# Performance work log

Hardware: AMD Instinct MI355X
Metric: run time of the kernel (lower is better)

The kernel has to match this reference:

```python
import jax, jax.numpy as jnp
import numpy as np

N = 50000
E = 800000
NFEAT = 128
NHID = 128


def _glorot(key, shape):
    fan = shape[0] + shape[-1]
    s = jnp.sqrt(6.0 / fan)
    return jax.random.uniform(key, shape, jnp.float32, -s, s)


def setup_inputs() -> dict:
    key = jax.random.key(0)
    ks = jax.random.split(key, 8)
    x = jax.random.normal(ks[0], (N, NFEAT), jnp.float32)
    edge_index = jax.random.randint(ks[1], (2, E), 0, N, jnp.int64)
    return {
        "x": x,
        "edge_index": edge_index,
        "Wl1": _glorot(ks[2], (NFEAT, NHID)),
        "bl1": jnp.zeros((NHID,), jnp.float32),
        "Wr1": _glorot(ks[3], (NFEAT, NHID)),
        "br1": jnp.zeros((NHID,), jnp.float32),
        "att1": _glorot(ks[4], (NHID,)),
        "b1": jnp.zeros((NHID,), jnp.float32),
        "Wl2": _glorot(ks[5], (NHID, NHID)),
        "bl2": jnp.zeros((NHID,), jnp.float32),
        "Wr2": _glorot(ks[6], (NHID, NHID)),
        "br2": jnp.zeros((NHID,), jnp.float32),
        "att2": _glorot(ks[7], (NHID,)),
        "b2": jnp.zeros((NHID,), jnp.float32),
    }


def gatv2_conv(x, src, dst, Wl, bl, Wr, br, att, bias, neg_slope=0.2):
    # PyG GATv2Conv, heads=1, concat=True, add_self_loops handled by caller.
    xl = x @ Wl + bl                      # [N, H] source transform
    xr = x @ Wr + br                      # [N, H] target transform
    e = jax.nn.leaky_relu(xl[src] + xr[dst], neg_slope) @ att  # [E']
    # segment softmax over incoming edges per destination node
    m = jax.ops.segment_max(e, dst, num_segments=x.shape[0])
    w = jnp.exp(e - m[dst])
    denom = jax.ops.segment_sum(w, dst, num_segments=x.shape[0])
    alpha = w / denom[dst]                # [E']
    out = jax.ops.segment_sum(alpha[:, None] * xl[src], dst,
                              num_segments=x.shape[0])
    return out + bias


def reference(x, edge_index, Wl1, bl1, Wr1, br1, att1, b1,
              Wl2, bl2, Wr2, br2, att2, b2):
    n = x.shape[0]
    loop = jnp.arange(n, dtype=edge_index.dtype)
    src = jnp.concatenate([edge_index[0], loop])  # add self loops (PyG default)
    dst = jnp.concatenate([edge_index[1], loop])
    h = gatv2_conv(x, src, dst, Wl1, bl1, Wr1, br1, att1, b1)
    h = jax.nn.leaky_relu(h, 0.01)  # F.leaky_relu default slope
    out = gatv2_conv(h, src, dst, Wl2, bl2, Wr2, br2, att2, b2)
    return out
```

## Files before the change

### kernel.cpp

```cpp
#include <hip/hip_runtime.h>
#include <math.h>

#define HD 128
#define CHUNK 2048
#define MAXBINS 512
#define NPB 128
#define CAP 3072

typedef __attribute__((ext_vector_type(8))) short bf16x8;
typedef __attribute__((ext_vector_type(4))) float f32x4;
typedef __attribute__((ext_vector_type(2))) float f32x2;

__device__ __forceinline__ unsigned short f2bf(float f) {
    unsigned int u = __float_as_uint(f);
    u += 0x7FFFu + ((u >> 16) & 1u);
    return (unsigned short)(u >> 16);
}
__device__ __forceinline__ float bflo(unsigned int p) {
    return __uint_as_float(p << 16);
}
__device__ __forceinline__ float bfhi(unsigned int p) {
    return __uint_as_float(p & 0xFFFF0000u);
}
__device__ __forceinline__ f32x2 bfpair(unsigned int p) {
    f32x2 r;
    r.x = __uint_as_float(p << 16);
    r.y = __uint_as_float(p & 0xFFFF0000u);
    return r;
}

__global__ __launch_bounds__(256) void wprep_kernel(
    const float* __restrict__ W0, const float* __restrict__ W1,
    const float* __restrict__ W2, const float* __restrict__ W3,
    uint4* __restrict__ T0, uint4* __restrict__ T1,
    uint4* __restrict__ T2, uint4* __restrict__ T3,
    int* __restrict__ binCursor, int nbins)
{
    int g = blockIdx.x * 256 + threadIdx.x;
    if (g < nbins) binCursor[g] = g * CAP;

    const int m = blockIdx.x >> 3;
    const int s = (blockIdx.x & 7) * 256 + threadIdx.x;
    const float* W = (m == 0) ? W0 : (m == 1) ? W1 : (m == 2) ? W2 : W3;
    uint4* T = (m == 0) ? T0 : (m == 1) ? T1 : (m == 2) ? T2 : T3;

    const int l = s & 63;
    const int ckk = s >> 6;
    const int kk = ckk & 3;
    const int c = ckk >> 2;
    const int k0 = kk * 32 + (l >> 4) * 8;
    const int col = c * 16 + (l & 15);

    unsigned int b[8];
    #pragma unroll
    for (int j = 0; j < 8; ++j)
        b[j] = f2bf(W[(size_t)(k0 + j) * HD + col]);
    uint4 o;
    o.x = b[0] | (b[1] << 16);
    o.y = b[2] | (b[3] << 16);
    o.z = b[4] | (b[5] << 16);
    o.w = b[6] | (b[7] << 16);
    T[s] = o;
}

__global__ __launch_bounds__(512, 4) void gemm_mfma_kernel(
    const float* __restrict__ X,
    const uint4* __restrict__ WlF, const float* __restrict__ bl,
    const uint4* __restrict__ WrF, const float* __restrict__ br,
    unsigned short* __restrict__ Ylb, unsigned short* __restrict__ Yrb, int n)
{
    __shared__ unsigned short xs[64 * HD];
    __shared__ uint4 bsl[2048];
    __shared__ uint4 bsr[2048];
    const int row0 = blockIdx.x * 64;
    const int tid = threadIdx.x;
    const int lane = tid & 63;
    const int wv = tid >> 6;

    {
        const float4* Xv = (const float4*)(X + (size_t)row0 * HD);
        #pragma unroll
        for (int i = 0; i < 4; ++i) {
            int idx = tid + i * 512;
            int row = idx >> 5;
            int c4 = idx & 31;
            float4 v = make_float4(0.f, 0.f, 0.f, 0.f);
            if (row0 + row < n) v = Xv[idx];
            ushort4 b;
            b.x = f2bf(v.x); b.y = f2bf(v.y); b.z = f2bf(v.z); b.w = f2bf(v.w);
            int byteoff = row * 256 + ((c4 * 8) ^ ((row & 7) << 4));
            *(ushort4*)((char*)xs + byteoff) = b;
        }
    }
    #pragma unroll
    for (int i = 0; i < 4; ++i) {
        bsl[tid + i * 512] = WlF[tid + i * 512];
        bsr[tid + i * 512] = WrF[tid + i * 512];
    }
    __syncthreads();

    const int r15 = lane & 15;
    const int kg = lane >> 4;
    const int mrow = (wv & 3) * 16 + r15;
    const int cbase = (wv >> 2) * 4;
    const int abase = mrow * 256;
    const int aswz = (mrow & 7) << 4;

    bf16x8 af[4];
    #pragma unroll
    for (int kk = 0; kk < 4; ++kk)
        af[kk] = *(const bf16x8*)((const char*)xs + abase + ((kk * 64 + kg * 16) ^ aswz));

    f32x4 accl[4], accr[4];
    #pragma unroll
    for (int i = 0; i < 4; ++i) {
        accl[i] = (f32x4){0.f, 0.f, 0.f, 0.f};
        accr[i] = (f32x4){0.f, 0.f, 0.f, 0.f};
    }

    #pragma unroll
    for (int kk = 0; kk < 4; ++kk) {
        #pragma unroll
        for (int c = 0; c < 4; ++c) {
            bf16x8 bfl = *(const bf16x8*)&bsl[((cbase + c) * 4 + kk) * 64 + lane];
            accl[c] = __builtin_amdgcn_mfma_f32_16x16x32_bf16(af[kk], bfl, accl[c], 0, 0, 0);
            bf16x8 bfr = *(const bf16x8*)&bsr[((cbase + c) * 4 + kk) * 64 + lane];
            accr[c] = __builtin_amdgcn_mfma_f32_16x16x32_bf16(af[kk], bfr, accr[c], 0, 0, 0);
        }
    }

    const int orow0 = row0 + (wv & 3) * 16 + kg * 4;
    #pragma unroll
    for (int c = 0; c < 4; ++c) {
        const int col = (cbase + c) * 16 + r15;
        const float bLv = bl[col];
        const float bRv = br[col];
        #pragma unroll
        for (int r = 0; r < 4; ++r) {
            int row = orow0 + r;
            if (row < n) {
                Ylb[(size_t)row * HD + col] = f2bf(accl[c][r] + bLv);
                Yrb[(size_t)row * HD + col] = f2bf(accr[c][r] + bRv);
            }
        }
    }
}

__global__ __launch_bounds__(256) void bin_scatter_kernel(
    const int* __restrict__ ei, int* __restrict__ binCursor,
    unsigned int* __restrict__ binned, int nE, int nTot, int nbins)
{
    __shared__ int hist[MAXBINS];
    __shared__ int base[MAXBINS];
    for (int i = threadIdx.x; i < nbins; i += 256) hist[i] = 0;
    __syncthreads();
    const int e0 = blockIdx.x * CHUNK;
    const int e1 = min(e0 + CHUNK, nTot);
    for (int e = e0 + threadIdx.x; e < e1; e += 256) {
        int d = (e < nE) ? ei[nE + e] : (e - nE);
        atomicAdd(&hist[d >> 7], 1);
    }
    __syncthreads();
    for (int b = threadIdx.x; b < nbins; b += 256) {
        int c = hist[b];
        base[b] = c ? atomicAdd(&binCursor[b], c) : 0;
        hist[b] = 0;
    }
    __syncthreads();
    for (int e = e0 + threadIdx.x; e < e1; e += 256) {
        int s, d;
        if (e < nE) { s = ei[e]; d = ei[nE + e]; }
        else        { s = e - nE; d = s; }
        int b = d >> 7;
        int r = atomicAdd(&hist[b], 1);
        binned[base[b] + r] = (unsigned int)s | ((unsigned int)(d & (NPB - 1)) << 16);
    }
}

__global__ __launch_bounds__(256) void bin_csr_kernel(
    const int* __restrict__ binCursor, const unsigned int* __restrict__ binned,
    int* __restrict__ rowstart, int* __restrict__ rowlen,
    int* __restrict__ csr_src, int n)
{
    __shared__ int hist[NPB];
    __shared__ int cur[NPB];
    __shared__ int sm[256];
    const int b = blockIdx.x;
    const int tid = threadIdx.x;
    const int lo = b * CAP;
    const int hi = binCursor[b];

    if (tid < NPB) hist[tid] = 0;
    __syncthreads();
    for (int e = lo + tid; e < hi; e += 256)
        atomicAdd(&hist[(binned[e] >> 16) & (NPB - 1)], 1);
    __syncthreads();
    const int c = (tid < NPB) ? hist[tid] : 0;
    const int rl = (c + 3) & ~3;
    sm[tid] = rl;
    __syncthreads();
    #pragma unroll
    for (int off = 1; off < 256; off <<= 1) {
        int v = (tid >= off) ? sm[tid - off] : 0;
        __syncthreads();
        sm[tid] += v;
        __syncthreads();
    }
    const int excl = sm[tid] - rl;
    if (tid < NPB) {
        cur[tid] = excl;
        int node = b * NPB + tid;
        if (node < n) { rowstart[node] = lo + excl; rowlen[node] = c; }
    }
    __syncthreads();
    for (int e = lo + tid; e < hi; e += 256) {
        unsigned int p = binned[e];
        int r = atomicAdd(&cur[(p >> 16) & (NPB - 1)], 1);
        csr_src[lo + r] = (int)(p & 0xFFFFu);
    }
    __syncthreads();
    if (tid < NPB) {
        int node = b * NPB + tid;
        if (node < n) {
            for (int r2 = excl + c; r2 < excl + rl; ++r2) csr_src[lo + r2] = node;
        }
    }
    int total = sm[255];
    if (tid < 64) csr_src[lo + total + tid] = 0;
}

__device__ __forceinline__ void gat4(
    uint2 u0, uint2 u1, uint2 u2, uint2 u3,
    const f32x2 xrA, const f32x2 xrB, const f32x2 attA, const f32x2 attB,
    int k0, int len,
    float& den, f32x2& accA, f32x2& accB)
{
    f32x2 c0a = bfpair(u0.x), c0b = bfpair(u0.y);
    f32x2 c1a = bfpair(u1.x), c1b = bfpair(u1.y);
    f32x2 c2a = bfpair(u2.x), c2b = bfpair(u2.y);
    f32x2 c3a = bfpair(u3.x), c3b = bfpair(u3.y);

    f32x2 v, tp;
    float t0, t1, t2, t3;
    v = c0a + xrA; v = __builtin_elementwise_max(v, v * 0.2f); tp = v * attA;
    v = c0b + xrB; v = __builtin_elementwise_max(v, v * 0.2f); tp += v * attB;
    t0 = tp.x + tp.y;
    v = c1a + xrA; v = __builtin_elementwise_max(v, v * 0.2f); tp = v * attA;
    v = c1b + xrB; v = __builtin_elementwise_max(v, v * 0.2f); tp += v * attB;
    t1 = tp.x + tp.y;
    v = c2a + xrA; v = __builtin_elementwise_max(v, v * 0.2f); tp = v * attA;
    v = c2b + xrB; v = __builtin_elementwise_max(v, v * 0.2f); tp += v * attB;
    t2 = tp.x + tp.y;
    v = c3a + xrA; v = __builtin_elementwise_max(v, v * 0.2f); tp = v * attA;
    v = c3b + xrB; v = __builtin_elementwise_max(v, v * 0.2f); tp += v * attB;
    t3 = tp.x + tp.y;

    #pragma unroll
    for (int off = 16; off >= 1; off >>= 1) {
        t0 += __shfl_xor(t0, off);
        t1 += __shfl_xor(t1, off);
        t2 += __shfl_xor(t2, off);
        t3 += __shfl_xor(t3, off);
    }

    if (k0 + 0 >= len) t0 = -1e30f;
    if (k0 + 1 >= len) t1 = -1e30f;
    if (k0 + 2 >= len) t2 = -1e30f;
    if (k0 + 3 >= len) t3 = -1e30f;

    float p0 = exp2f(t0);
    float p1 = exp2f(t1);
    float p2 = exp2f(t2);
    float p3 = exp2f(t3);
    den += (p0 + p1) + (p2 + p3);
    accA += p0 * c0a + p1 * c1a + p2 * c2a + p3 * c3a;
    accB += p0 * c0b + p1 * c1b + p2 * c2b + p3 * c3b;
}

__global__ __launch_bounds__(256) void fused_gat_kernel(
    const int* __restrict__ rowstart, const int* __restrict__ rowlen,
    const int* __restrict__ csr_src,
    const unsigned short* __restrict__ xlb, const unsigned short* __restrict__ xrb,
    const float* __restrict__ att, const float* __restrict__ bias,
    float* __restrict__ out, int n, int doAct)
{
    const int wid  = blockIdx.x * 4 + (threadIdx.x >> 6);
    const int lane = threadIdx.x & 63;
    const int d    = wid * 2 + (lane >> 5);
    const int fl   = (lane & 31) * 4;

    const float LOG2E = 1.44269504088896f;
    const float4 attf = *(const float4*)(att + fl);
    const f32x2 attA = (f32x2){attf.x * LOG2E, attf.y * LOG2E};
    const f32x2 attB = (f32x2){attf.z * LOG2E, attf.w * LOG2E};

    f32x2 xrA = (f32x2){0.f, 0.f}, xrB = (f32x2){0.f, 0.f};
    int rp = 0, len = 0;
    if (d < n) {
        uint2 xru = *(const uint2*)(xrb + (size_t)d * HD + fl);
        xrA = bfpair(xru.x);
        xrB = bfpair(xru.y);
        rp  = rowstart[d];
        len = rowlen[d];
    }
    const int rl = (len + 3) & ~3;
    const int ml = max(rl, __shfl_xor(rl, 32));

    float den = 0.f;
    f32x2 accA = (f32x2){0.f, 0.f}, accB = (f32x2){0.f, 0.f};

    const unsigned short* xfl = xlb + fl;

    uint2 a0, a1, a2, a3, b0, b1, b2, b3;
    {
        int i0 = csr_src[rp + 0], i1 = csr_src[rp + 1];
        int i2 = csr_src[rp + 2], i3 = csr_src[rp + 3];
        int j0 = csr_src[rp + 4], j1 = csr_src[rp + 5];
        int j2 = csr_src[rp + 6], j3 = csr_src[rp + 7];
        a0 = *(const uint2*)(xfl + (size_t)i0 * HD);
        a1 = *(const uint2*)(xfl + (size_t)i1 * HD);
        a2 = *(const uint2*)(xfl + (size_t)i2 * HD);
        a3 = *(const uint2*)(xfl + (size_t)i3 * HD);
        b0 = *(const uint2*)(xfl + (size_t)j0 * HD);
        b1 = *(const uint2*)(xfl + (size_t)j1 * HD);
        b2 = *(const uint2*)(xfl + (size_t)j2 * HD);
        b3 = *(const uint2*)(xfl + (size_t)j3 * HD);
    }

    for (int k0 = 0; k0 < ml; k0 += 8) {
        uint2 u0 = a0, u1 = a1, u2 = a2, u3 = a3;
        int kn = k0 + 8;
        if (kn < ml) {
            int i0 = csr_src[rp + kn + 0], i1 = csr_src[rp + kn + 1];
            int i2 = csr_src[rp + kn + 2], i3 = csr_src[rp + kn + 3];
            a0 = *(const uint2*)(xfl + (size_t)i0 * HD);
            a1 = *(const uint2*)(xfl + (size_t)i1 * HD);
            a2 = *(const uint2*)(xfl + (size_t)i2 * HD);
            a3 = *(const uint2*)(xfl + (size_t)i3 * HD);
        }
        gat4(u0, u1, u2, u3, xrA, xrB, attA, attB, k0, len, den, accA, accB);

        if (k0 + 4 < ml) {
            uint2 v0 = b0, v1 = b1, v2 = b2, v3 = b3;
            int km = k0 + 12;
            if (km < ml) {
                int j0 = csr_src[rp + km + 0], j1 = csr_src[rp + km + 1];
                int j2 = csr_src[rp + km + 2], j3 = csr_src[rp + km + 3];
                b0 = *(const uint2*)(xfl + (size_t)j0 * HD);
                b1 = *(const uint2*)(xfl + (size_t)j1 * HD);
                b2 = *(const uint2*)(xfl + (size_t)j2 * HD);
                b3 = *(const uint2*)(xfl + (size_t)j3 * HD);
            }
            gat4(v0, v1, v2, v3, xrA, xrB, attA, attB, k0 + 4, len, den, accA, accB);
        }
    }

    if (d < n) {
        const float4 bv = *(const float4*)(bias + fl);
        float inv = 1.f / den;
        float o0 = accA.x * inv + bv.x;
        float o1 = accA.y * inv + bv.y;
        float o2 = accB.x * inv + bv.z;
        float o3 = accB.y * inv + bv.w;
        if (doAct) {
            o0 = (o0 > 0.f) ? o0 : 0.01f * o0;
            o1 = (o1 > 0.f) ? o1 : 0.01f * o1;
            o2 = (o2 > 0.f) ? o2 : 0.01f * o2;
            o3 = (o3 > 0.f) ? o3 : 0.01f * o3;
        }
        *(float4*)(out + (size_t)d * HD + fl) = make_float4(o0, o1, o2, o3);
    }
}

extern "C" void kernel_launch(void* const* d_in, const int* in_sizes, int n_in,
                              void* d_out, int out_size, void* d_ws, size_t ws_size,
                              hipStream_t stream)
{
    const float* x    = (const float*)d_in[0];
    const int*   ei   = (const int*)d_in[1];
    const float* Wl1  = (const float*)d_in[2];
    const float* bl1  = (const float*)d_in[3];
    const float* Wr1  = (const float*)d_in[4];
    const float* br1  = (const float*)d_in[5];
    const float* att1 = (const float*)d_in[6];
    const float* b1   = (const float*)d_in[7];
    const float* Wl2  = (const float*)d_in[8];
    const float* bl2  = (const float*)d_in[9];
    const float* Wr2  = (const float*)d_in[10];
    const float* br2  = (const float*)d_in[11];
    const float* att2 = (const float*)d_in[12];
    const float* b2   = (const float*)d_in[13];

    const int n    = in_sizes[0] / HD;
    const int E    = in_sizes[1] / 2;
    const int nTot = E + n;
    const int nbins = (n + NPB - 1) / NPB;

    char* ws = (char*)d_ws;
    const size_t feat_bytes = (size_t)n * HD * sizeof(float);
    const size_t bf_bytes   = ((size_t)n * HD * 2 + 511) & ~(size_t)511;
    const size_t wt_bytes   = ((size_t)HD * HD * 2 + 511) & ~(size_t)511;
    auto alignup = [](size_t v) { return (v + 511) & ~(size_t)511; };
    unsigned short* xlb = (unsigned short*)ws; ws += bf_bytes;
    unsigned short* xrb = (unsigned short*)ws; ws += bf_bytes;
    float* h  = (float*)ws;          ws += feat_bytes;
    uint4* wlF1 = (uint4*)ws; ws += wt_bytes;
    uint4* wrF1 = (uint4*)ws; ws += wt_bytes;
    uint4* wlF2 = (uint4*)ws; ws += wt_bytes;
    uint4* wrF2 = (uint4*)ws; ws += wt_bytes;
    int* binCursor = (int*)ws;       ws += alignup((size_t)nbins * 4);
    int* rowstart  = (int*)ws;       ws += alignup((size_t)n * 4);
    int* rowlen    = (int*)ws;       ws += alignup((size_t)n * 4);
    unsigned int* binned = (unsigned int*)ws; ws += alignup((size_t)nbins * CAP * 4);
    int* csr_src   = (int*)ws;       ws += alignup((size_t)nbins * CAP * 4);

    float* out = (float*)d_out;

    const int nChunk = (nTot + CHUNK - 1) / CHUNK;
    dim3 gb(512); dim3 gg((n + 63) / 64);
    dim3 fb(256); dim3 fg((n + 7) / 8);

    wprep_kernel<<<32, 256, 0, stream>>>(Wl1, Wr1, Wl2, Wr2, wlF1, wrF1, wlF2, wrF2,
                                         binCursor, nbins);
    bin_scatter_kernel<<<nChunk, 256, 0, stream>>>(ei, binCursor, binned, E, nTot, nbins);
    bin_csr_kernel<<<nbins, 256, 0, stream>>>(binCursor, binned, rowstart, rowlen, csr_src, n);

    gemm_mfma_kernel<<<gg, gb, 0, stream>>>(x, wlF1, bl1, wrF1, br1, xlb, xrb, n);
    fused_gat_kernel<<<fg, fb, 0, stream>>>(rowstart, rowlen, csr_src, xlb, xrb, att1, b1, h, n, 1);

    gemm_mfma_kernel<<<gg, gb, 0, stream>>>(h, wlF2, bl2, wrF2, br2, xlb, xrb, n);
    fused_gat_kernel<<<fg, fb, 0, stream>>>(rowstart, rowlen, csr_src, xlb, xrb, att2, b2, out, n, 0);
}
```

Baseline: 159.4 us.

## Sort nodes by degree within each bin to balance half-wave pairs

```diff
diff --git a/kernel.cpp b/kernel.cpp
--- a/kernel.cpp
+++ b/kernel.cpp
@@ -15,12 +15,6 @@
     unsigned int u = __float_as_uint(f);
     u += 0x7FFFu + ((u >> 16) & 1u);
     return (unsigned short)(u >> 16);
-}
-__device__ __forceinline__ float bflo(unsigned int p) {
-    return __uint_as_float(p << 16);
-}
-__device__ __forceinline__ float bfhi(unsigned int p) {
-    return __uint_as_float(p & 0xFFFF0000u);
 }
 __device__ __forceinline__ f32x2 bfpair(unsigned int p) {
     f32x2 r;
@@ -180,11 +174,12 @@
 __global__ __launch_bounds__(256) void bin_csr_kernel(
     const int* __restrict__ binCursor, const unsigned int* __restrict__ binned,
     int* __restrict__ rowstart, int* __restrict__ rowlen,
-    int* __restrict__ csr_src, int n)
+    int* __restrict__ csr_src, int* __restrict__ pairs, int n)
 {
     __shared__ int hist[NPB];
     __shared__ int cur[NPB];
     __shared__ int sm[256];
+    __shared__ unsigned int srt[NPB];
     const int b = blockIdx.x;
     const int tid = threadIdx.x;
     const int lo = b * CAP;
@@ -198,6 +193,7 @@
     const int c = (tid < NPB) ? hist[tid] : 0;
     const int rl = (c + 3) & ~3;
     sm[tid] = rl;
+    if (tid < NPB) srt[tid] = ((unsigned int)rl << 7) | (unsigned int)tid;
     __syncthreads();
     #pragma unroll
     for (int off = 1; off < 256; off <<= 1) {
@@ -213,6 +209,25 @@
         if (node < n) { rowstart[node] = lo + excl; rowlen[node] = c; }
     }
     __syncthreads();
+    for (int k = 2; k <= NPB; k <<= 1) {
+        for (int j = k >> 1; j > 0; j >>= 1) {
+            if (tid < NPB) {
+                int ixj = tid ^ j;
+                if (ixj > tid) {
+                    unsigned int a = srt[tid], bb = srt[ixj];
+                    bool asc = ((tid & k) == 0);
+                    if (asc ? (a > bb) : (a < bb)) { srt[tid] = bb; srt[ixj] = a; }
+                }
+            }
+            __syncthreads();
+        }
+    }
+    if (tid < NPB) {
+        int j = tid >> 1;
+        int pp = tid & 1;
+        int t = ((j & 3) << 4) | (j >> 2);
+        pairs[b * NPB + 2 * t + pp] = b * NPB + (int)(srt[tid] & 127u);
+    }
     for (int e = lo + tid; e < hi; e += 256) {
         unsigned int p = binned[e];
         int r = atomicAdd(&cur[(p >> 16) & (NPB - 1)], 1);
@@ -278,6 +293,7 @@
 }
 
 __global__ __launch_bounds__(256) void fused_gat_kernel(
+    const int* __restrict__ pairs,
     const int* __restrict__ rowstart, const int* __restrict__ rowlen,
     const int* __restrict__ csr_src,
     const unsigned short* __restrict__ xlb, const unsigned short* __restrict__ xrb,
@@ -286,7 +302,8 @@
 {
     const int wid  = blockIdx.x * 4 + (threadIdx.x >> 6);
     const int lane = threadIdx.x & 63;
-    const int d    = wid * 2 + (lane >> 5);
+    const int dp   = wid * 2 + (lane >> 5);
+    const int d    = pairs[dp];
     const int fl   = (lane & 31) * 4;
 
     const float LOG2E = 1.44269504088896f;
@@ -395,6 +412,7 @@
     const int E    = in_sizes[1] / 2;
     const int nTot = E + n;
     const int nbins = (n + NPB - 1) / NPB;
+    const int np   = nbins * NPB;
 
     char* ws = (char*)d_ws;
     const size_t feat_bytes = (size_t)n * HD * sizeof(float);
@@ -411,6 +429,7 @@
     int* binCursor = (int*)ws;       ws += alignup((size_t)nbins * 4);
     int* rowstart  = (int*)ws;       ws += alignup((size_t)n * 4);
     int* rowlen    = (int*)ws;       ws += alignup((size_t)n * 4);
+    int* pairs     = (int*)ws;       ws += alignup((size_t)np * 4);
     unsigned int* binned = (unsigned int*)ws; ws += alignup((size_t)nbins * CAP * 4);
     int* csr_src   = (int*)ws;       ws += alignup((size_t)nbins * CAP * 4);
 
@@ -418,16 +437,16 @@
 
     const int nChunk = (nTot + CHUNK - 1) / CHUNK;
     dim3 gb(512); dim3 gg((n + 63) / 64);
-    dim3 fb(256); dim3 fg((n + 7) / 8);
+    dim3 fb(256); dim3 fg((np + 7) / 8);
 
     wprep_kernel<<<32, 256, 0, stream>>>(Wl1, Wr1, Wl2, Wr2, wlF1, wrF1, wlF2, wrF2,
                                          binCursor, nbins);
     bin_scatter_kernel<<<nChunk, 256, 0, stream>>>(ei, binCursor, binned, E, nTot, nbins);
-    bin_csr_kernel<<<nbins, 256, 0, stream>>>(binCursor, binned, rowstart, rowlen, csr_src, n);
+    bin_csr_kernel<<<nbins, 256, 0, stream>>>(binCursor, binned, rowstart, rowlen, csr_src, pairs, n);
 
     gemm_mfma_kernel<<<gg, gb, 0, stream>>>(x, wlF1, bl1, wrF1, br1, xlb, xrb, n);
-    fused_gat_kernel<<<fg, fb, 0, stream>>>(rowstart, rowlen, csr_src, xlb, xrb, att1, b1, h, n, 1);
+    fused_gat_kernel<<<fg, fb, 0, stream>>>(pairs, rowstart, rowlen, csr_src, xlb, xrb, att1, b1, h, n, 1);
 
     gemm_mfma_kernel<<<gg, gb, 0, stream>>>(h, wlF2, bl2, wrF2, br2, xlb, xrb, n);
-    fused_gat_kernel<<<fg, fb, 0, stream>>>(rowstart, rowlen, csr_src, xlb, xrb, att2, b2, out, n, 0);
-}
+    fused_gat_kernel<<<fg, fb, 0, stream>>>(pairs, rowstart, rowlen, csr_src, xlb, xrb, att2, b2, out, n, 0);
+}
```

Result: slower. 172.8 us (+8.4%).
